# Performance work log

Hardware: AMD Instinct MI355X
Metric: run time of the kernel (lower is better)

The kernel has to match this reference:

```python
import jax, jax.numpy as jnp
import numpy as np

B, T, C = 8, 2048, 1024
N_HEAD = 16
HEAD_DIM = C // N_HEAD  # 64


def setup_inputs() -> dict:
    key = jax.random.key(0)
    k1, k2, k3 = jax.random.split(key, 3)
    x = jax.random.normal(k1, (B, T, C), dtype=jnp.float32)
    # qkv projection: Linear(C, 3*head_dim) with bias
    W = jax.random.normal(k2, (C, 3 * HEAD_DIM), dtype=jnp.float32) * (1.0 / np.sqrt(C))
    b = jax.random.normal(k3, (3 * HEAD_DIM,), dtype=jnp.float32) * 0.01
    return {"x": x, "W": W, "b": b}


def reference(x, W, b):
    # qkv projection, then chunk into (k, q, v) -- note key comes first in the original
    kqv = x @ W + b                       # [B, T, 3*hd]
    k, q, v = jnp.split(kqv, 3, axis=-1)  # each [B, T, hd]
    scale = HEAD_DIM ** -0.5
    wei = jnp.einsum('bth,bsh->bts', q, k) * scale  # [B, T, T]
    t = x.shape[1]
    causal = jnp.tril(jnp.ones((t, t), dtype=bool))
    wei = jnp.where(causal, wei, -jnp.inf)
    wei = jax.nn.softmax(wei, axis=-1)
    # dropout p=0.0 -> identity
    out = jnp.einsum('bts,bsh->bth', wei, v)  # [B, T, hd]
    return out
```

## Files before the change

### kernel.cpp

```cpp
#include <hip/hip_runtime.h>

#define NB 8
#define NT 2048
#define NC 1024
#define HD 64
#define N3 192

typedef float f32x4 __attribute__((ext_vector_type(4)));
typedef _Float16 f16x8 __attribute__((ext_vector_type(8)));
typedef short short8 __attribute__((ext_vector_type(8)));
typedef short short4v __attribute__((ext_vector_type(4)));

static __device__ __forceinline__ short f2h(float f) {
  _Float16 h = (_Float16)f;
  return __builtin_bit_cast(short, h);
}

typedef __attribute__((address_space(1))) const void* gptr1;
typedef __attribute__((address_space(3))) void* sptr3;
static __device__ __forceinline__ void gload_lds16(const void* g, void* s) {
  __builtin_amdgcn_global_load_lds((gptr1)g, (sptr3)s, 16, 0, 0);
}

__launch_bounds__(256)
__global__ void prep_w(const float* __restrict__ W, short* __restrict__ Wt) {
  const int n = blockIdx.x;
  for (int k = threadIdx.x; k < NC; k += 256) {
    Wt[(size_t)n * NC + k] = f2h(W[(size_t)k * N3 + n]);
  }
}

__launch_bounds__(256, 2)
__global__ void qkv_proj(const float* __restrict__ x, const short* __restrict__ Wt,
                         const float* __restrict__ bias, short* __restrict__ Kb,
                         short* __restrict__ Qb, short* __restrict__ Vt,
                         float* __restrict__ kmax2) {
  __shared__ short Ax[2][32 * 64];
  __shared__ short Bw[2][192 * 64];

  const int tid = threadIdx.x;
  const int lane = tid & 63;
  const int wave = tid >> 6;
  const int wr = wave >> 1, wc = wave & 1;
  const int r0 = blockIdx.x * 32;
  const int batch = r0 >> 11;
  const int t0 = r0 & (NT - 1);
  const int g = lane >> 4, c = lane & 15;

  const int bsub = lane >> 3;
  const size_t bgoff = (size_t)bsub * (NC * 2) + (size_t)((lane & 7) ^ bsub) * 16;

  f32x4 acc[6];
#pragma unroll
  for (int nt = 0; nt < 6; ++nt) acc[nt] = (f32x4){0.f, 0.f, 0.f, 0.f};

  float4 areg[2];

  auto stage_B = [&](int kt, int p) {
    const char* src = (const char*)Wt + (size_t)(wave * 48) * (NC * 2) +
                      (size_t)kt * 128 + bgoff;
    char* dst = (char*)Bw[p] + wave * 48 * 128;
#pragma unroll
    for (int j = 0; j < 6; ++j)
      gload_lds16(src + (size_t)(j * 8) * (NC * 2), dst + j * 8 * 128);
  };
  auto load_A = [&](int kt) {
    const float* xp = x + (size_t)r0 * NC + kt * 64;
#pragma unroll
    for (int i = 0; i < 2; ++i) {
      int idx = tid + 256 * i;
      int row = idx >> 4, c4 = idx & 15;
      areg[i] = *(const float4*)(xp + (size_t)row * NC + c4 * 4);
    }
  };
  auto write_A = [&](int p) {
#pragma unroll
    for (int i = 0; i < 2; ++i) {
      int idx = tid + 256 * i;
      int row = idx >> 4, c4 = idx & 15;
      int byte = row * 128 + ((c4 * 8) ^ ((row & 7) << 4));
      float4 v = areg[i];
      short4v h;
      h[0] = f2h(v.x); h[1] = f2h(v.y); h[2] = f2h(v.z); h[3] = f2h(v.w);
      *(short4v*)((char*)Ax[p] + byte) = h;
    }
  };
  auto compute = [&](int p) {
#pragma unroll
    for (int kc = 0; kc < 2; ++kc) {
      const int arow = wr * 16 + c;
      f16x8 a = *(const f16x8*)((const char*)Ax[p] + arow * 128 +
                                ((kc * 64 + (g << 4)) ^ ((arow & 7) << 4)));
#pragma unroll
      for (int nt = 0; nt < 6; ++nt) {
        const int brow = wc * 96 + nt * 16 + c;
        f16x8 b = *(const f16x8*)((const char*)Bw[p] + brow * 128 +
                                  ((kc * 64 + (g << 4)) ^ ((brow & 7) << 4)));
        acc[nt] = __builtin_amdgcn_mfma_f32_16x16x32_f16(a, b, acc[nt], 0, 0, 0);
      }
    }
  };

  stage_B(0, 0);
  load_A(0);
  write_A(0);
  __syncthreads();
#pragma unroll 1
  for (int kt = 0; kt < 16; ++kt) {
    const int p = kt & 1;
    if (kt < 15) { stage_B(kt + 1, p ^ 1); load_A(kt + 1); }
    compute(p);
    if (kt < 15) write_A(p ^ 1);
    __syncthreads();
  }

  float bv[6];
#pragma unroll
  for (int nt = 0; nt < 6; ++nt) bv[nt] = bias[wc * 96 + nt * 16 + c];

  short* VTl = (short*)Ax[0];
  float knorm[4] = {0.f, 0.f, 0.f, 0.f};
#pragma unroll
  for (int nt = 0; nt < 6; ++nt) {
#pragma unroll
    for (int i = 0; i < 4; ++i) {
      int n = wc * 96 + nt * 16 + c;
      int lrow = wr * 16 + (g << 2) + i;
      float v = acc[nt][i] + bv[nt];
      size_t tok = ((size_t)batch << 11) | (size_t)(t0 + lrow);
      if (n < 64) {
        Kb[tok * HD + n] = f2h(v);
        knorm[i] += v * v;
      } else if (n < 128) {
        Qb[tok * HD + (n - 64)] = f2h(v);
      } else {
        int h = n - 128;
        int byte = h * 64 + ((lrow * 2) ^ ((h & 3) << 4));
        *(short*)((char*)VTl + byte) = f2h(v);
      }
    }
  }
  if (wc == 0) {
#pragma unroll
    for (int d = 1; d < 16; d <<= 1)
#pragma unroll
      for (int i = 0; i < 4; ++i) knorm[i] += __shfl_xor(knorm[i], d);
    float mx = fmaxf(fmaxf(knorm[0], knorm[1]), fmaxf(knorm[2], knorm[3]));
    if (c == 0) atomicMax((int*)(kmax2 + batch), __float_as_int(mx));
  }
  __syncthreads();
  {
    int h = tid >> 2, ch = tid & 3;
    short8 v = *(const short8*)((const char*)VTl + h * 64 +
                                ((ch * 16) ^ ((h & 3) << 4)));
    *(short8*)(Vt + (((size_t)(batch * HD + h)) << 11) + (size_t)t0 + ch * 8) = v;
  }
}

__launch_bounds__(64)
__global__ void attn(const short* __restrict__ Kb, const short* __restrict__ Qb,
                     const short* __restrict__ Vt, const float* __restrict__ kmax2,
                     float* __restrict__ out) {
  __shared__ short Vlds[2][64 * 64];
  __shared__ short Ones[16 * 64];
  __shared__ short Plds[32 * 64];

  const int lane = threadIdx.x;
  const int g = lane >> 4, c = lane & 15;
  const int qt = blockIdx.x & 63;
  const int batch = blockIdx.x >> 6;
  const int q0 = qt * 32;
  const int nkv = (qt >> 1) + 1;
  const float c2 = 0.125f * 1.44269504088896340736f;

#pragma unroll
  for (int i = 0; i < 16; ++i) {
    int idx = lane + 64 * i;
    Ones[idx] = (i == 0) ? (short)0x3C00 : (short)0;
  }

  f16x8 qa[2][2];
#pragma unroll
  for (int mt = 0; mt < 2; ++mt) {
    size_t base = (((size_t)batch << 11) | (size_t)(q0 + mt * 16 + c)) * HD + (g << 3);
    qa[mt][0] = *(const f16x8*)(Qb + base);
    qa[mt][1] = *(const f16x8*)(Qb + base + 32);
  }
  float m2r[2][4];
  {
    const float kmaxn = sqrtf(kmax2[batch]);
#pragma unroll
    for (int mt = 0; mt < 2; ++mt) {
      float qn = 0.f;
#pragma unroll
      for (int kc = 0; kc < 2; ++kc)
#pragma unroll
        for (int j = 0; j < 8; ++j) {
          float qv = (float)qa[mt][kc][j];
          qn += qv * qv;
        }
      qn += __shfl_xor(qn, 16);
      qn += __shfl_xor(qn, 32);
#pragma unroll
      for (int i = 0; i < 4; ++i)
        m2r[mt][i] = sqrtf(__shfl(qn, (g << 2) + i)) * kmaxn * c2;
    }
  }

  f32x4 o[2][5];
#pragma unroll
  for (int mt = 0; mt < 2; ++mt)
#pragma unroll
    for (int nt = 0; nt < 5; ++nt) o[mt][nt] = (f32x4){0.f, 0.f, 0.f, 0.f};

  f16x8 kfr[4][2];
  const short* kbp = Kb + (((size_t)batch << 11)) * HD;
  auto load_K = [&](int t) {
    const short* kp = kbp + (size_t)(t * 64) * HD;
#pragma unroll
    for (int st = 0; st < 4; ++st) {
      size_t rb = (size_t)(st * 16 + c) * HD + (g << 3);
      kfr[st][0] = *(const f16x8*)(kp + rb);
      kfr[st][1] = *(const f16x8*)(kp + rb + 32);
    }
  };
  const int vsub = lane >> 3;
  const size_t vgoff = (size_t)vsub * (NT * 2) + (size_t)((lane & 7) ^ vsub) * 16;
  const char* vbase = (const char*)(Vt + (((size_t)batch * HD) << 11));
  auto stage_V = [&](int t, int p) {
    const char* src = vbase + (size_t)t * 128 + vgoff;
    char* dst = (char*)Vlds[p];
#pragma unroll
    for (int j = 0; j < 8; ++j)
      gload_lds16(src + (size_t)(j * 8) * (NT * 2), dst + j * 8 * 128);
  };

  stage_V(0, 0);
  load_K(0);
  int p = 0;
#pragma unroll 1
  for (int t = 0; t < nkv; ++t) {
    const int s0 = t * 64;
    if (t + 1 < nkv) stage_V(t + 1, p ^ 1);

    f32x4 s[2][4];
#pragma unroll
    for (int mt = 0; mt < 2; ++mt)
#pragma unroll
      for (int st = 0; st < 4; ++st) s[mt][st] = (f32x4){0.f, 0.f, 0.f, 0.f};
#pragma unroll
    for (int kc = 0; kc < 2; ++kc)
#pragma unroll
      for (int st = 0; st < 4; ++st) {
        s[0][st] = __builtin_amdgcn_mfma_f32_16x16x32_f16(qa[0][kc], kfr[st][kc], s[0][st], 0, 0, 0);
        s[1][st] = __builtin_amdgcn_mfma_f32_16x16x32_f16(qa[1][kc], kfr[st][kc], s[1][st], 0, 0, 0);
      }

    if (t + 1 < nkv) load_K(t + 1);

    const bool diag = (s0 + 63 > q0);
#pragma unroll
    for (int mt = 0; mt < 2; ++mt)
#pragma unroll
      for (int st = 0; st < 4; ++st)
#pragma unroll
        for (int i = 0; i < 4; ++i) {
          int cg = s0 + st * 16 + c;
          int rg = q0 + mt * 16 + (g << 2) + i;
          float pv = __builtin_amdgcn_exp2f(s[mt][st][i] * c2 - m2r[mt][i]);
          if (diag && cg > rg) pv = 0.f;
          int prow = mt * 16 + (g << 2) + i;
          *(short*)((char*)Plds + prow * 128 +
                    (((st * 16 + c) * 2) ^ ((prow & 7) << 4))) = f2h(pv);
        }

    asm volatile("s_waitcnt vmcnt(0)" ::: "memory");
    __builtin_amdgcn_sched_barrier(0);

#pragma unroll
    for (int kc = 0; kc < 2; ++kc) {
      f16x8 pa[2];
#pragma unroll
      for (int mt = 0; mt < 2; ++mt) {
        int prow = mt * 16 + c;
        pa[mt] = *(const f16x8*)((const char*)Plds + prow * 128 +
                                 ((kc * 64 + (g << 4)) ^ ((prow & 7) << 4)));
      }
#pragma unroll
      for (int nt = 0; nt < 5; ++nt) {
        f16x8 b;
        if (nt < 4) {
          int vrow = nt * 16 + c;
          b = *(const f16x8*)((const char*)Vlds[p] + vrow * 128 +
                              ((kc * 64 + (g << 4)) ^ ((vrow & 7) << 4)));
        } else {
          b = *(const f16x8*)((const char*)Ones + c * 128 + kc * 64 + (g << 4));
        }
        o[0][nt] = __builtin_amdgcn_mfma_f32_16x16x32_f16(pa[0], b, o[0][nt], 0, 0, 0);
        o[1][nt] = __builtin_amdgcn_mfma_f32_16x16x32_f16(pa[1], b, o[1][nt], 0, 0, 0);
      }
    }
    p ^= 1;
  }

#pragma unroll
  for (int mt = 0; mt < 2; ++mt)
#pragma unroll
    for (int i = 0; i < 4; ++i) {
      float l = __shfl(o[mt][4][i], (lane >> 4) << 4);
      float inv = 1.0f / l;
      int rg = q0 + mt * 16 + (g << 2) + i;
#pragma unroll
      for (int nt = 0; nt < 4; ++nt)
        out[(((size_t)batch << 11) | (size_t)rg) * HD + nt * 16 + c] = o[mt][nt][i] * inv;
    }
}

extern "C" void kernel_launch(void* const* d_in, const int* in_sizes, int n_in,
                              void* d_out, int out_size, void* d_ws, size_t ws_size,
                              hipStream_t stream) {
  const float* x = (const float*)d_in[0];
  const float* W = (const float*)d_in[1];
  const float* bias = (const float*)d_in[2];
  float* out = (float*)d_out;

  char* ws = (char*)d_ws;
  float* kmax2 = (float*)ws;
  short* Wt = (short*)(ws + 256);
  short* Kb = Wt + (size_t)N3 * NC;
  short* Qb = Kb + (size_t)NB * NT * HD;
  short* Vt = Qb + (size_t)NB * NT * HD;

  hipMemsetAsync(kmax2, 0, 8 * sizeof(float), stream);
  prep_w<<<N3, 256, 0, stream>>>(W, Wt);
  qkv_proj<<<512, 256, 0, stream>>>(x, Wt, bias, Kb, Qb, Vt, kmax2);
  attn<<<NB * 64, 64, 0, stream>>>(Kb, Qb, Vt, kmax2, out);
}
```

Before: 173.1 us.

## Split causal attention over KV chunks with 4-wave blocks and combine kernel

Replaces the single-wave attention kernel with a 256-thread kernel that splits each 64-row query tile's KV range into four chunks. K and V tiles are staged into shared LDS by async loads, and partial outputs and row sums go to a workspace. A second kernel adds the partials and normalizes. This is meant to balance the causal triangle's uneven work and raise occupancy, but it costs an extra launch and a round trip of partial results through global memory. The weight-transpose prep kernel is also rewritten to use vectorized stores.

```diff
diff --git a/kernel.cpp b/kernel.cpp
--- a/kernel.cpp
+++ b/kernel.cpp
@@ -24,10 +24,16 @@
 
 __launch_bounds__(256)
 __global__ void prep_w(const float* __restrict__ W, short* __restrict__ Wt) {
-  const int n = blockIdx.x;
-  for (int k = threadIdx.x; k < NC; k += 256) {
-    Wt[(size_t)n * NC + k] = f2h(W[(size_t)k * N3 + n]);
-  }
+  const int n = threadIdx.x;
+  if (n >= 192) return;
+  const int k0 = blockIdx.x * 16;
+  short8 v0, v1;
+#pragma unroll
+  for (int j = 0; j < 8; ++j) v0[j] = f2h(W[(size_t)(k0 + j) * N3 + n]);
+#pragma unroll
+  for (int j = 0; j < 8; ++j) v1[j] = f2h(W[(size_t)(k0 + 8 + j) * N3 + n]);
+  *(short8*)(Wt + (size_t)n * NC + k0) = v0;
+  *(short8*)(Wt + (size_t)n * NC + k0 + 8) = v1;
 }
 
 __launch_bounds__(256, 2)
@@ -157,163 +163,172 @@
   }
 }
 
-__launch_bounds__(64)
-__global__ void attn(const short* __restrict__ Kb, const short* __restrict__ Qb,
-                     const short* __restrict__ Vt, const float* __restrict__ kmax2,
-                     float* __restrict__ out) {
-  __shared__ short Vlds[2][64 * 64];
-  __shared__ short Ones[16 * 64];
-  __shared__ short Plds[32 * 64];
-
-  const int lane = threadIdx.x;
+__launch_bounds__(256)
+__global__ void attn_part(const short* __restrict__ Kb, const short* __restrict__ Qb,
+                          const short* __restrict__ Vt, const float* __restrict__ kmax2,
+                          float* __restrict__ Opart, float* __restrict__ Lpart) {
+  __shared__ short Kld[2][64 * 64];
+  __shared__ short Vld[2][64 * 64];
+  __shared__ short Pld[4][16 * 64];
+
+  const int tid = threadIdx.x, lane = tid & 63, wave = tid >> 6;
   const int g = lane >> 4, c = lane & 15;
-  const int qt = blockIdx.x & 63;
-  const int batch = blockIdx.x >> 6;
-  const int q0 = qt * 32;
-  const int nkv = (qt >> 1) + 1;
+  const int bid = blockIdx.x;
+  const int ch = bid & 3;
+  const int qt = 31 - ((bid >> 2) & 31);
+  const int b = bid >> 7;
+  const int nkv = qt + 1;
+  const int ks = ch * nkv / 4, ke = (ch + 1) * nkv / 4;
+  if (ks == ke) return;
+  const int q0 = qt * 64;
+  const int slot = (b * 32 + qt) * 4 + ch;
   const float c2 = 0.125f * 1.44269504088896340736f;
 
-#pragma unroll
-  for (int i = 0; i < 16; ++i) {
-    int idx = lane + 64 * i;
-    Ones[idx] = (i == 0) ? (short)0x3C00 : (short)0;
-  }
-
-  f16x8 qa[2][2];
-#pragma unroll
-  for (int mt = 0; mt < 2; ++mt) {
-    size_t base = (((size_t)batch << 11) | (size_t)(q0 + mt * 16 + c)) * HD + (g << 3);
-    qa[mt][0] = *(const f16x8*)(Qb + base);
-    qa[mt][1] = *(const f16x8*)(Qb + base + 32);
-  }
-  float m2r[2][4];
+  f16x8 qa[2];
   {
-    const float kmaxn = sqrtf(kmax2[batch]);
-#pragma unroll
-    for (int mt = 0; mt < 2; ++mt) {
-      float qn = 0.f;
-#pragma unroll
-      for (int kc = 0; kc < 2; ++kc)
-#pragma unroll
-        for (int j = 0; j < 8; ++j) {
-          float qv = (float)qa[mt][kc][j];
-          qn += qv * qv;
-        }
-      qn += __shfl_xor(qn, 16);
-      qn += __shfl_xor(qn, 32);
-#pragma unroll
-      for (int i = 0; i < 4; ++i)
-        m2r[mt][i] = sqrtf(__shfl(qn, (g << 2) + i)) * kmaxn * c2;
-    }
-  }
-
-  f32x4 o[2][5];
-#pragma unroll
-  for (int mt = 0; mt < 2; ++mt)
-#pragma unroll
-    for (int nt = 0; nt < 5; ++nt) o[mt][nt] = (f32x4){0.f, 0.f, 0.f, 0.f};
-
-  f16x8 kfr[4][2];
-  const short* kbp = Kb + (((size_t)batch << 11)) * HD;
-  auto load_K = [&](int t) {
-    const short* kp = kbp + (size_t)(t * 64) * HD;
-#pragma unroll
-    for (int st = 0; st < 4; ++st) {
-      size_t rb = (size_t)(st * 16 + c) * HD + (g << 3);
-      kfr[st][0] = *(const f16x8*)(kp + rb);
-      kfr[st][1] = *(const f16x8*)(kp + rb + 32);
-    }
-  };
-  const int vsub = lane >> 3;
-  const size_t vgoff = (size_t)vsub * (NT * 2) + (size_t)((lane & 7) ^ vsub) * 16;
-  const char* vbase = (const char*)(Vt + (((size_t)batch * HD) << 11));
-  auto stage_V = [&](int t, int p) {
-    const char* src = vbase + (size_t)t * 128 + vgoff;
-    char* dst = (char*)Vlds[p];
-#pragma unroll
-    for (int j = 0; j < 8; ++j)
-      gload_lds16(src + (size_t)(j * 8) * (NT * 2), dst + j * 8 * 128);
-  };
-
-  stage_V(0, 0);
-  load_K(0);
+    size_t qbase = ((size_t)b * NT + (size_t)(q0 + wave * 16 + c)) * HD + (g << 3);
+    qa[0] = *(const f16x8*)(Qb + qbase);
+    qa[1] = *(const f16x8*)(Qb + qbase + 32);
+  }
+  float m2r[4];
+  {
+    const float kmaxn = sqrtf(kmax2[b]);
+    float qn = 0.f;
+#pragma unroll
+    for (int kc = 0; kc < 2; ++kc)
+#pragma unroll
+      for (int j = 0; j < 8; ++j) {
+        float qv = (float)qa[kc][j];
+        qn += qv * qv;
+      }
+    qn += __shfl_xor(qn, 16);
+    qn += __shfl_xor(qn, 32);
+#pragma unroll
+    for (int i = 0; i < 4; ++i)
+      m2r[i] = sqrtf(__shfl(qn, (g << 2) + i)) * kmaxn * c2;
+  }
+
+  f32x4 o[5];
+#pragma unroll
+  for (int nt = 0; nt < 5; ++nt) o[nt] = (f32x4){0.f, 0.f, 0.f, 0.f};
+  f16x8 bone;
+#pragma unroll
+  for (int j = 0; j < 8; ++j) bone[j] = (c == 0) ? (_Float16)1.0f : (_Float16)0.0f;
+
+  const int sub = lane >> 3, chx = (lane & 7) ^ sub;
+  const char* ksrc = (const char*)Kb + ((size_t)b * NT) * 128;
+  const char* vsrc = (const char*)Vt + ((size_t)b * HD) * 4096;
+
+  auto stage = [&](int t, int p) {
+    const int s0 = t * 64;
+    const char* kp = ksrc + (size_t)(s0 + wave * 16 + sub) * 128 + (size_t)chx * 16;
+    const char* vp = vsrc + (size_t)(wave * 16 + sub) * 4096 + (size_t)s0 * 2 + (size_t)chx * 16;
+    gload_lds16(kp, (char*)Kld[p] + (wave * 16) * 128);
+    gload_lds16(kp + 8 * 128, (char*)Kld[p] + (wave * 16 + 8) * 128);
+    gload_lds16(vp, (char*)Vld[p] + (wave * 16) * 128);
+    gload_lds16(vp + (size_t)8 * 4096, (char*)Vld[p] + (wave * 16 + 8) * 128);
+  };
+
+  stage(ks, 0);
+  __syncthreads();
   int p = 0;
 #pragma unroll 1
-  for (int t = 0; t < nkv; ++t) {
+  for (int t = ks; t < ke; ++t) {
+    if (t + 1 < ke) stage(t + 1, p ^ 1);
     const int s0 = t * 64;
-    if (t + 1 < nkv) stage_V(t + 1, p ^ 1);
-
-    f32x4 s[2][4];
-#pragma unroll
-    for (int mt = 0; mt < 2; ++mt)
-#pragma unroll
-      for (int st = 0; st < 4; ++st) s[mt][st] = (f32x4){0.f, 0.f, 0.f, 0.f};
+
+    f32x4 s[4];
+#pragma unroll
+    for (int st = 0; st < 4; ++st) s[st] = (f32x4){0.f, 0.f, 0.f, 0.f};
 #pragma unroll
     for (int kc = 0; kc < 2; ++kc)
 #pragma unroll
       for (int st = 0; st < 4; ++st) {
-        s[0][st] = __builtin_amdgcn_mfma_f32_16x16x32_f16(qa[0][kc], kfr[st][kc], s[0][st], 0, 0, 0);
-        s[1][st] = __builtin_amdgcn_mfma_f32_16x16x32_f16(qa[1][kc], kfr[st][kc], s[1][st], 0, 0, 0);
-      }
-
-    if (t + 1 < nkv) load_K(t + 1);
-
-    const bool diag = (s0 + 63 > q0);
-#pragma unroll
-    for (int mt = 0; mt < 2; ++mt)
-#pragma unroll
-      for (int st = 0; st < 4; ++st)
-#pragma unroll
-        for (int i = 0; i < 4; ++i) {
-          int cg = s0 + st * 16 + c;
-          int rg = q0 + mt * 16 + (g << 2) + i;
-          float pv = __builtin_amdgcn_exp2f(s[mt][st][i] * c2 - m2r[mt][i]);
-          if (diag && cg > rg) pv = 0.f;
-          int prow = mt * 16 + (g << 2) + i;
-          *(short*)((char*)Plds + prow * 128 +
-                    (((st * 16 + c) * 2) ^ ((prow & 7) << 4))) = f2h(pv);
-        }
-
-    asm volatile("s_waitcnt vmcnt(0)" ::: "memory");
-    __builtin_amdgcn_sched_barrier(0);
+        int row = st * 16 + c;
+        f16x8 bk = *(const f16x8*)((const char*)Kld[p] + row * 128 +
+                                   ((kc * 64 + (g << 4)) ^ ((row & 7) << 4)));
+        s[st] = __builtin_amdgcn_mfma_f32_16x16x32_f16(qa[kc], bk, s[st], 0, 0, 0);
+      }
+
+    const bool diag = (t == qt);
+#pragma unroll
+    for (int st = 0; st < 4; ++st)
+#pragma unroll
+      for (int i = 0; i < 4; ++i) {
+        float pv = __builtin_amdgcn_exp2f(s[st][i] * c2 - m2r[i]);
+        if (diag && (s0 + st * 16 + c) > (q0 + wave * 16 + (g << 2) + i)) pv = 0.f;
+        int prow = (g << 2) + i;
+        *(short*)((char*)Pld[wave] + prow * 128 +
+                  (((st * 16 + c) * 2) ^ ((prow & 7) << 4))) = f2h(pv);
+      }
 
 #pragma unroll
     for (int kc = 0; kc < 2; ++kc) {
-      f16x8 pa[2];
-#pragma unroll
-      for (int mt = 0; mt < 2; ++mt) {
-        int prow = mt * 16 + c;
-        pa[mt] = *(const f16x8*)((const char*)Plds + prow * 128 +
-                                 ((kc * 64 + (g << 4)) ^ ((prow & 7) << 4)));
-      }
-#pragma unroll
-      for (int nt = 0; nt < 5; ++nt) {
-        f16x8 b;
-        if (nt < 4) {
-          int vrow = nt * 16 + c;
-          b = *(const f16x8*)((const char*)Vlds[p] + vrow * 128 +
-                              ((kc * 64 + (g << 4)) ^ ((vrow & 7) << 4)));
-        } else {
-          b = *(const f16x8*)((const char*)Ones + c * 128 + kc * 64 + (g << 4));
-        }
-        o[0][nt] = __builtin_amdgcn_mfma_f32_16x16x32_f16(pa[0], b, o[0][nt], 0, 0, 0);
-        o[1][nt] = __builtin_amdgcn_mfma_f32_16x16x32_f16(pa[1], b, o[1][nt], 0, 0, 0);
-      }
-    }
+      f16x8 pa = *(const f16x8*)((const char*)Pld[wave] + c * 128 +
+                                 ((kc * 64 + (g << 4)) ^ ((c & 7) << 4)));
+#pragma unroll
+      for (int nt = 0; nt < 4; ++nt) {
+        int vrow = nt * 16 + c;
+        f16x8 bv = *(const f16x8*)((const char*)Vld[p] + vrow * 128 +
+                                   ((kc * 64 + (g << 4)) ^ ((vrow & 7) << 4)));
+        o[nt] = __builtin_amdgcn_mfma_f32_16x16x32_f16(pa, bv, o[nt], 0, 0, 0);
+      }
+      o[4] = __builtin_amdgcn_mfma_f32_16x16x32_f16(pa, bone, o[4], 0, 0, 0);
+    }
+    __syncthreads();
     p ^= 1;
   }
 
-#pragma unroll
-  for (int mt = 0; mt < 2; ++mt)
-#pragma unroll
-    for (int i = 0; i < 4; ++i) {
-      float l = __shfl(o[mt][4][i], (lane >> 4) << 4);
-      float inv = 1.0f / l;
-      int rg = q0 + mt * 16 + (g << 2) + i;
-#pragma unroll
-      for (int nt = 0; nt < 4; ++nt)
-        out[(((size_t)batch << 11) | (size_t)rg) * HD + nt * 16 + c] = o[mt][nt][i] * inv;
-    }
+  float* ob = Opart + (size_t)slot * 4096 + (size_t)(wave * 16) * 64;
+#pragma unroll
+  for (int i = 0; i < 4; ++i) {
+    int r = (g << 2) + i;
+#pragma unroll
+    for (int nt = 0; nt < 4; ++nt) ob[r * 64 + nt * 16 + c] = o[nt][i];
+  }
+  if (c == 0) {
+#pragma unroll
+    for (int i = 0; i < 4; ++i)
+      Lpart[slot * 64 + wave * 16 + (g << 2) + i] = o[4][i];
+  }
+}
+
+__launch_bounds__(256)
+__global__ void attn_comb(const float* __restrict__ Opart, const float* __restrict__ Lpart,
+                          float* __restrict__ out) {
+  const int qt = blockIdx.x & 31;
+  const int b = blockIdx.x >> 5;
+  const int nkv = qt + 1;
+  const int t = threadIdx.x;
+  const int base = (b * 32 + qt) * 4;
+
+  f32x4 acc[4];
+  float lsum[4];
+#pragma unroll
+  for (int j = 0; j < 4; ++j) { acc[j] = (f32x4){0.f, 0.f, 0.f, 0.f}; lsum[j] = 0.f; }
+
+#pragma unroll
+  for (int ch = 0; ch < 4; ++ch) {
+    int ks = ch * nkv / 4, ke = (ch + 1) * nkv / 4;
+    if (ks == ke) continue;
+    const float* op = Opart + (size_t)(base + ch) * 4096;
+    const float* lp = Lpart + (base + ch) * 64;
+#pragma unroll
+    for (int j = 0; j < 4; ++j) {
+      int row = (t >> 4) + 16 * j;
+      acc[j] += *(const f32x4*)(op + row * 64 + (t & 15) * 4);
+      lsum[j] += lp[row];
+    }
+  }
+  float* ob = out + ((size_t)b * NT + (size_t)qt * 64) * HD;
+#pragma unroll
+  for (int j = 0; j < 4; ++j) {
+    int row = (t >> 4) + 16 * j;
+    float inv = 1.0f / lsum[j];
+    f32x4 v = acc[j];
+    v[0] *= inv; v[1] *= inv; v[2] *= inv; v[3] *= inv;
+    *(f32x4*)(ob + row * 64 + (t & 15) * 4) = v;
+  }
 }
 
 extern "C" void kernel_launch(void* const* d_in, const int* in_sizes, int n_in,
@@ -330,9 +345,12 @@
   short* Kb = Wt + (size_t)N3 * NC;
   short* Qb = Kb + (size_t)NB * NT * HD;
   short* Vt = Qb + (size_t)NB * NT * HD;
+  float* Opart = (float*)(Vt + (size_t)NB * NT * HD);
+  float* Lpart = Opart + (size_t)1024 * 4096;
 
   hipMemsetAsync(kmax2, 0, 8 * sizeof(float), stream);
-  prep_w<<<N3, 256, 0, stream>>>(W, Wt);
+  prep_w<<<64, 256, 0, stream>>>(W, Wt);
   qkv_proj<<<512, 256, 0, stream>>>(x, Wt, bias, Kb, Qb, Vt, kmax2);
-  attn<<<NB * 64, 64, 0, stream>>>(Kb, Qb, Vt, kmax2, out);
-}
+  attn_part<<<NB * 32 * 4, 256, 0, stream>>>(Kb, Qb, Vt, kmax2, Opart, Lpart);
+  attn_comb<<<NB * 32, 256, 0, stream>>>(Opart, Lpart, out);
+}
```

Result: faster. 141.8 us (-18.1%).
